# Kernel optimization log

Measured on AMD Instinct MI355X. Metric: run time of the kernel, lower is better.

Reference implementation:

```python
import jax, jax.numpy as jnp
import numpy as np

KERNEL_SIZE = 9
HEAD_SIZE = 64


def setup_inputs() -> dict:
    key = jax.random.key(0)
    k1, k2 = jax.random.split(key)
    B, S, D = 8, 4096, 768          # hidden = num_heads(12) * head_size(64)
    H = D // HEAD_SIZE              # 12 heads
    inputs = jax.random.normal(k1, (B, S, D), dtype=jnp.float32)
    filters = jax.random.normal(k2, (B, S, H * KERNEL_SIZE), dtype=jnp.float32)
    return {"inputs": inputs, "filters": filters}


def reference(inputs, filters):
    k = KERNEL_SIZE
    hd = HEAD_SIZE
    bs, S, d = inputs.shape
    H = d // hd
    pad = k // 2
    # softmax-normalized per-(position, head) kernels: [B, S, H, k]
    f = jax.nn.softmax(filters.reshape(bs, S, H, k), axis=-1)
    # 'same' padding along sequence, then gather sliding windows (im2col)
    x = jnp.pad(inputs, ((0, 0), (pad, pad), (0, 0)))        # [B, S+k-1, d]
    idx = jnp.arange(S)[:, None] + jnp.arange(k)[None, :]     # [S, k]
    win = x[:, idx].reshape(bs, S, k, H, hd)                  # [B, S, k, H, hd]
    # dynamic depthwise conv: contract kernel taps per head
    out = jnp.einsum('bskhd,bshk->bshd', win, f)              # [B, S, H, hd]
    return out
```

## Files before the change

kernel.cpp:

```cpp
#include <hip/hip_runtime.h>
#include <math.h>


#define KS 9
#define HD 64
#define NH 12
#define DMODEL 768
#define SEQ 4096
#define BATCH 8
#define TTILE 32
#define CHUNKS (SEQ / TTILE)

__global__ __launch_bounds__(192, 4) void lightconv_kernel(
    const float* __restrict__ x,
    const float* __restrict__ filt,
    float* __restrict__ out)
{
    const int blk   = blockIdx.x;
    const int chunk = blk & (CHUNKS - 1);
    const int b     = blk / CHUNKS;
    const int s0    = chunk * TTILE;
    const int t     = threadIdx.x;
    const int head  = t >> 4;
    const int d4    = (t & 15) << 2;

    const float*  xc = x   + (size_t)b * SEQ * DMODEL + head * HD + d4;
    float*        oc = out + (size_t)b * SEQ * DMODEL + head * HD + d4;
    const float*  fc = filt + (size_t)b * SEQ * (NH * KS) + head * KS;

    const float4 zero = make_float4(0.f, 0.f, 0.f, 0.f);

    float4 win[KS];
#pragma unroll
    for (int k = 0; k < KS - 1; ++k) {
        const int ss = s0 + k - (KS / 2);
        win[k] = (ss >= 0) ? *reinterpret_cast<const float4*>(xc + (size_t)ss * DMODEL) : zero;
    }

#pragma unroll
    for (int i = 0; i < TTILE; ++i) {
        const int s  = s0 + i;
        const int ss = s + (KS / 2);
        win[KS - 1] = (ss < SEQ) ? *reinterpret_cast<const float4*>(xc + (size_t)ss * DMODEL)
                                 : zero;

        const float* fp = fc + (size_t)s * (NH * KS);
        float w[KS];
        float m = -1e30f;
#pragma unroll
        for (int k = 0; k < KS; ++k) { w[k] = fp[k]; m = fmaxf(m, w[k]); }
        float sum = 0.f;
#pragma unroll
        for (int k = 0; k < KS; ++k) { w[k] = __expf(w[k] - m); sum += w[k]; }
        const float inv = 1.0f / sum;

        float4 acc = zero;
#pragma unroll
        for (int k = 0; k < KS; ++k) {
            const float wk = w[k] * inv;
            acc.x += wk * win[k].x;
            acc.y += wk * win[k].y;
            acc.z += wk * win[k].z;
            acc.w += wk * win[k].w;
        }
        *reinterpret_cast<float4*>(oc + (size_t)s * DMODEL) = acc;

#pragma unroll
        for (int k = 0; k < KS - 1; ++k) win[k] = win[k + 1];
    }
}

extern "C" void kernel_launch(void* const* d_in, const int* in_sizes, int n_in,
                              void* d_out, int out_size, void* d_ws, size_t ws_size,
                              hipStream_t stream) {
    const float* x    = (const float*)d_in[0];
    const float* filt = (const float*)d_in[1];
    float* out        = (float*)d_out;

    const int grid = BATCH * CHUNKS;
    lightconv_kernel<<<grid, 192, 0, stream>>>(x, filt, out);
}
```

Measured before the change: 204.2 us.

## Stage filter tile in LDS and compute softmax once per position-head

Each block now loads its whole filter tile into shared memory with coalesced loads, and each (position, head) pair's softmax is computed once by one thread and written back normalized. Previously every one of the 16 threads per head recomputed the same softmax from scattered global loads. The tile is halved to 16 positions and the occupancy hint is raised to give more blocks. The cost is two barriers per block and extra halo reloads of x from the smaller tile.

```diff
diff --git a/kernel.cpp b/kernel.cpp
--- a/kernel.cpp
+++ b/kernel.cpp
@@ -8,25 +8,54 @@
 #define DMODEL 768
 #define SEQ 4096
 #define BATCH 8
-#define TTILE 32
+#define TTILE 16
 #define CHUNKS (SEQ / TTILE)
+#define FSTRIDE (NH * KS)
+#define NTHREADS 192
 
-__global__ __launch_bounds__(192, 4) void lightconv_kernel(
+__global__ __launch_bounds__(NTHREADS, 6) void lightconv_kernel(
     const float* __restrict__ x,
     const float* __restrict__ filt,
     float* __restrict__ out)
 {
+    __shared__ float wlds[TTILE * FSTRIDE];
+
     const int blk   = blockIdx.x;
     const int chunk = blk & (CHUNKS - 1);
-    const int b     = blk / CHUNKS;
+    const int b     = blk >> 8;
     const int s0    = chunk * TTILE;
     const int t     = threadIdx.x;
-    const int head  = t >> 4;
-    const int d4    = (t & 15) << 2;
 
-    const float*  xc = x   + (size_t)b * SEQ * DMODEL + head * HD + d4;
-    float*        oc = out + (size_t)b * SEQ * DMODEL + head * HD + d4;
-    const float*  fc = filt + (size_t)b * SEQ * (NH * KS) + head * KS;
+    const float* fbase = filt + ((size_t)b * SEQ + s0) * FSTRIDE;
+#pragma unroll
+    for (int i = 0; i < (TTILE * FSTRIDE) / NTHREADS; ++i) {
+        const int idx = t + i * NTHREADS;
+        wlds[idx] = fbase[idx];
+    }
+    __syncthreads();
+
+    {
+        const int sl = t & 15;
+        const int hh = t >> 4;
+        float* wp = &wlds[sl * FSTRIDE + hh * KS];
+        float w[KS];
+        float m = -1e30f;
+#pragma unroll
+        for (int k = 0; k < KS; ++k) { w[k] = wp[k]; m = fmaxf(m, w[k]); }
+        float sum = 0.f;
+#pragma unroll
+        for (int k = 0; k < KS; ++k) { w[k] = __expf(w[k] - m); sum += w[k]; }
+        const float inv = 1.0f / sum;
+#pragma unroll
+        for (int k = 0; k < KS; ++k) wp[k] = w[k] * inv;
+    }
+    __syncthreads();
+
+    const int head = t >> 4;
+    const int d4   = (t & 15) << 2;
+
+    const float* xc = x   + (size_t)b * SEQ * DMODEL + head * HD + d4;
+    float*       oc = out + (size_t)b * SEQ * DMODEL + head * HD + d4;
 
     const float4 zero = make_float4(0.f, 0.f, 0.f, 0.f);
 
@@ -34,7 +63,8 @@
 #pragma unroll
     for (int k = 0; k < KS - 1; ++k) {
         const int ss = s0 + k - (KS / 2);
-        win[k] = (ss >= 0) ? *reinterpret_cast<const float4*>(xc + (size_t)ss * DMODEL) : zero;
+        win[k] = (ss >= 0) ? *reinterpret_cast<const float4*>(xc + (size_t)ss * DMODEL)
+                           : zero;
     }
 
 #pragma unroll
@@ -44,20 +74,12 @@
         win[KS - 1] = (ss < SEQ) ? *reinterpret_cast<const float4*>(xc + (size_t)ss * DMODEL)
                                  : zero;
 
-        const float* fp = fc + (size_t)s * (NH * KS);
-        float w[KS];
-        float m = -1e30f;
-#pragma unroll
-        for (int k = 0; k < KS; ++k) { w[k] = fp[k]; m = fmaxf(m, w[k]); }
-        float sum = 0.f;
-#pragma unroll
-        for (int k = 0; k < KS; ++k) { w[k] = __expf(w[k] - m); sum += w[k]; }
-        const float inv = 1.0f / sum;
+        const float* wp = &wlds[i * FSTRIDE + head * KS];
 
         float4 acc = zero;
 #pragma unroll
         for (int k = 0; k < KS; ++k) {
-            const float wk = w[k] * inv;
+            const float wk = wp[k];
             acc.x += wk * win[k].x;
             acc.y += wk * win[k].y;
             acc.z += wk * win[k].z;
@@ -78,5 +100,5 @@
     float* out        = (float*)d_out;
 
     const int grid = BATCH * CHUNKS;
-    lightconv_kernel<<<grid, 192, 0, stream>>>(x, filt, out);
+    lightconv_kernel<<<grid, NTHREADS, 0, stream>>>(x, filt, out);
 }
```

After: 192.7 us. 5.6% less time.

## Remap work to wave-per-sequence-tile with column thirds and reload windows each step

Applied to the files above, without the earlier changes.

Changes the work decomposition so each 256-thread block holds four waves, each covering 16 consecutive positions over a third of the model columns, giving many more blocks. Instead of a sliding register window, every position reloads all nine taps, relying on cache for reuse. Output stores become nontemporal. The aim is more occupancy and parallelism, at the cost of redundant global/cache loads and less register reuse.

```diff
diff --git a/kernel.cpp b/kernel.cpp
--- a/kernel.cpp
+++ b/kernel.cpp
@@ -8,43 +8,53 @@
 #define DMODEL 768
 #define SEQ 4096
 #define BATCH 8
-#define TTILE 32
-#define CHUNKS (SEQ / TTILE)
+#define FSTRIDE (NH * KS)
+#define L 16
+#define WPB 4
+#define NTHREADS 256
+#define NGROUPS (SEQ / (L * WPB))
+#define NBC (BATCH * 3)
+#define NBLOCKS (NGROUPS * NBC)
 
-__global__ __launch_bounds__(192, 4) void lightconv_kernel(
+typedef float f32x4 __attribute__((ext_vector_type(4)));
+
+__global__ __launch_bounds__(NTHREADS, 8) void lightconv_kernel(
     const float* __restrict__ x,
     const float* __restrict__ filt,
     float* __restrict__ out)
 {
-    const int blk   = blockIdx.x;
-    const int chunk = blk & (CHUNKS - 1);
-    const int b     = blk / CHUNKS;
-    const int s0    = chunk * TTILE;
-    const int t     = threadIdx.x;
-    const int head  = t >> 4;
-    const int d4    = (t & 15) << 2;
+    const int bid  = blockIdx.x;
+    const int G    = bid / NBC;
+    const int bc   = bid % NBC;
+    const int b    = bc / 3;
+    const int c    = bc % 3;
+    const int wav  = threadIdx.x >> 6;
+    const int lane = threadIdx.x & 63;
 
-    const float*  xc = x   + (size_t)b * SEQ * DMODEL + head * HD + d4;
-    float*        oc = out + (size_t)b * SEQ * DMODEL + head * HD + d4;
-    const float*  fc = filt + (size_t)b * SEQ * (NH * KS) + head * KS;
+    const int s0   = (G * WPB + wav) * L;
+    const int col4 = c * 64 + lane;
+    const int head = col4 >> 4;
 
-    const float4 zero = make_float4(0.f, 0.f, 0.f, 0.f);
+    const float* xc = x    + (size_t)b * SEQ * DMODEL + col4 * 4;
+    float*       oc = out  + (size_t)b * SEQ * DMODEL + col4 * 4;
+    const float* fc = filt + (size_t)b * SEQ * FSTRIDE + head * KS;
 
-    float4 win[KS];
+    const f32x4 zero = (f32x4)(0.f);
+
+#pragma unroll 1
+    for (int i = 0; i < L; ++i) {
+        const int s = s0 + i;
+
+        f32x4 win[KS];
 #pragma unroll
-    for (int k = 0; k < KS - 1; ++k) {
-        const int ss = s0 + k - (KS / 2);
-        win[k] = (ss >= 0) ? *reinterpret_cast<const float4*>(xc + (size_t)ss * DMODEL) : zero;
-    }
+        for (int k = 0; k < KS; ++k) {
+            const int ss = s + k - (KS / 2);
+            win[k] = ((unsigned)ss < (unsigned)SEQ)
+                   ? *reinterpret_cast<const f32x4*>(xc + (size_t)ss * DMODEL)
+                   : zero;
+        }
 
-#pragma unroll
-    for (int i = 0; i < TTILE; ++i) {
-        const int s  = s0 + i;
-        const int ss = s + (KS / 2);
-        win[KS - 1] = (ss < SEQ) ? *reinterpret_cast<const float4*>(xc + (size_t)ss * DMODEL)
-                                 : zero;
-
-        const float* fp = fc + (size_t)s * (NH * KS);
+        const float* fp = fc + (size_t)s * FSTRIDE;
         float w[KS];
         float m = -1e30f;
 #pragma unroll
@@ -54,19 +64,12 @@
         for (int k = 0; k < KS; ++k) { w[k] = __expf(w[k] - m); sum += w[k]; }
         const float inv = 1.0f / sum;
 
-        float4 acc = zero;
+        f32x4 acc = zero;
 #pragma unroll
         for (int k = 0; k < KS; ++k) {
-            const float wk = w[k] * inv;
-            acc.x += wk * win[k].x;
-            acc.y += wk * win[k].y;
-            acc.z += wk * win[k].z;
-            acc.w += wk * win[k].w;
+            acc += (w[k] * inv) * win[k];
         }
-        *reinterpret_cast<float4*>(oc + (size_t)s * DMODEL) = acc;
-
-#pragma unroll
-        for (int k = 0; k < KS - 1; ++k) win[k] = win[k + 1];
+        __builtin_nontemporal_store(acc, reinterpret_cast<f32x4*>(oc + (size_t)s * DMODEL));
     }
 }
 
@@ -77,6 +80,5 @@
     const float* filt = (const float*)d_in[1];
     float* out        = (float*)d_out;
 
-    const int grid = BATCH * CHUNKS;
-    lightconv_kernel<<<grid, 192, 0, stream>>>(x, filt, out);
+    lightconv_kernel<<<NBLOCKS, NTHREADS, 0, stream>>>(x, filt, out);
 }
```

After: 231.4 us. 13.3% more time.
